# Optimization experiments

Hardware: AMD Instinct MI355X
Metric: run time of the kernel (lower is better)

## Reference

```python
import jax, jax.numpy as jnp
import numpy as np

B = 16384      # samples
NN = 11        # causal-graph nodes per sample (adult)
D = 4          # per-node raw feature dim (node_dim_max)
F = 32         # dim_input_enc = h_dim_list_enc[0]
EDIM = 4       # edge_dim
NI = 3         # number of intervention features

_BASE_EDGES = np.array([[0,3],[0,4],[1,3],[1,5],[2,5],[0,6],[3,6],[4,7],[5,7],
                        [6,8],[7,8],[2,9],[8,9],[3,10],[6,10],[9,10],[1,10]], dtype=np.int64)


def setup_inputs() -> dict:
    key = jax.random.key(0)
    ks = jax.random.split(key, 14)
    # batched edge index: replicate the 17-edge DAG per sample with node offsets
    off = (np.arange(B) * NN)[:, None]                      # [B,1]
    src = (_BASE_EDGES[:, 0][None, :] + off).reshape(-1).astype(np.int32)  # [E]
    dst = (_BASE_EDGES[:, 1][None, :] + off).reshape(-1).astype(np.int32)
    E = src.shape[0]
    g = lambda k, shp, s: jax.random.normal(k, shp, dtype=jnp.float32) * s
    return {
        'x_input':  g(ks[0], (B, NN * D), 1.0),
        'edge_attr': g(ks[1], (E, EDIM), 1.0),
        'W_emb':   g(ks[2], (NN, D, F), 1.0 / np.sqrt(D)),
        'b_emb':   jnp.zeros((NN, F), jnp.float32),
        'W_pre1':  g(ks[3], (NI, 2 * F + EDIM, F), 1.0 / np.sqrt(2 * F + EDIM)),
        'b_pre1':  jnp.zeros((NI, F), jnp.float32),
        'W_post1': g(ks[4], (NI, 12 * F, F), 1.0 / np.sqrt(12 * F)),
        'b_post1': jnp.zeros((NI, F), jnp.float32),
        'W_pre2':  g(ks[5], (NI, 2 * F + EDIM, F), 1.0 / np.sqrt(2 * F + EDIM)),
        'b_pre2':  jnp.zeros((NI, F), jnp.float32),
        'W_post2': g(ks[6], (NI, 12 * F, 1), 1.0 / np.sqrt(12 * F)),
        'b_post2': jnp.zeros((NI, 1), jnp.float32),
        'W_fc':    g(ks[7], (NI, NN, 1), 1.0 / np.sqrt(NN)),
        'b_fc':    jnp.zeros((NI, 1), jnp.float32),
        'edge_src': jnp.asarray(src),
        'edge_dst': jnp.asarray(dst),
    }


def _pna_conv(h, src, dst, e, Wpre, bpre, Wpost, bpost, cnt_c, mask, amp, att, N):
    # message: pre-MLP over [h_dst, h_src, edge_attr]
    m = jax.nn.relu(jnp.concatenate([h[dst], h[src], e], axis=1) @ Wpre + bpre)  # [E,F]
    s = jax.ops.segment_sum(m, dst, num_segments=N)
    mean = s / cnt_c[:, None]
    mean_sq = jax.ops.segment_sum(m * m, dst, num_segments=N) / cnt_c[:, None]
    std = jnp.sqrt(jax.nn.relu(mean_sq - mean * mean) + 1e-5)
    mn = jnp.where(mask[:, None], jax.ops.segment_min(m, dst, num_segments=N), 0.0)
    mx = jnp.where(mask[:, None], jax.ops.segment_max(m, dst, num_segments=N), 0.0)
    agg = jnp.concatenate([mean, mn, mx, std], axis=1)                 # [N,4F]
    scaled = jnp.concatenate([agg, agg * amp[:, None], agg * att[:, None]], axis=1)  # [N,12F]
    return scaled @ Wpost + bpost


def reference(x_input, edge_attr, W_emb, b_emb,
              W_pre1, b_pre1, W_post1, b_post1,
              W_pre2, b_pre2, W_post2, b_post2,
              W_fc, b_fc, edge_src, edge_dst):
    N = B * NN
    # encoder embeddings: per-node linear + relu (shared across interventions)
    X = x_input.reshape(B, NN, D)
    H = jax.nn.relu(jnp.einsum('bnd,ndf->bnf', X, W_emb) + b_emb).reshape(N, F)
    # degree stats for PNA scalers (in-degree)
    cnt = jax.ops.segment_sum(jnp.ones_like(edge_dst, dtype=jnp.float32), edge_dst, num_segments=N)
    mask = cnt > 0
    cnt_c = jnp.maximum(cnt, 1.0)
    logd = jnp.log1p(jnp.maximum(cnt, 1.0))
    avg_log = jnp.mean(logd)
    amp = logd / avg_log
    att = avg_log / logd
    outs = []
    for i in range(NI):
        h1 = jax.nn.relu(_pna_conv(H, edge_src, edge_dst, edge_attr,
                                   W_pre1[i], b_pre1[i], W_post1[i], b_post1[i],
                                   cnt_c, mask, amp, att, N))
        h2 = _pna_conv(h1, edge_src, edge_dst, edge_attr,
                       W_pre2[i], b_pre2[i], W_post2[i], b_post2[i],
                       cnt_c, mask, amp, att, N)            # [N,1]
        p = jax.nn.sigmoid(h2)                               # get_prob=True
        pm = p.reshape(B, NN).mean(axis=0)                   # return_mean=True -> [11]
        outs.append(pm @ W_fc[i] + b_fc[i])                  # [1]
    # padded sum over interventions == concatenation when inter_features == intervention_features
    return jnp.concatenate(outs)[None, :]                    # [1, NI]
```

## Files before the change

kernel.cpp:

```cpp
#include <hip/hip_runtime.h>
#include <math.h>

#define B_TOT   16384
#define SB      5
#define TPB     512

#define SSTRIDE 1868
#define OFF_H   0
#define OFF_EA  396
#define OFF_M   464
#define OFF_H1  OFF_M
#define OFF_AGG 1076
#define OFF_TD  OFF_AGG
#define OFF_TS  (OFF_AGG + 396)
#define OFF_A4  600
#define OFF_A10 640
#define WLDS    (SB * SSTRIDE)

#define L_WC1  0
#define L_B4   3072
#define L_H1C  3104
#define L_V1C1 3136
#define L_V10  3232
#define L_V4   3360
#define L_C42  3392
#define LTAB   3396
#define G_W10  3396
#define G_W4   7492
#define WTAB   8520
#define WS_TAB 64
#define LDS_FLOATS (WLDS + LTAB)
#define AVG_LOG 0.9976091242438673f

__constant__ int C_ESRC[17] = {0,0,1,1,2,0,3,4,5,6,7,2,8,3,6,9,1};
__constant__ int C_EDST[17] = {3,4,3,5,5,6,6,7,7,8,8,9,9,10,10,10,10};
__constant__ int C1EA[6] = {0,3,5,7,9,11};
__constant__ int C1EB[6] = {2,4,6,8,10,12};
__constant__ int C1N[6]  = {3,5,6,7,8,9};
__constant__ int CC1[8]  = {0,0,1,2,3,4,5,0};

#define FMA16(a, wb, u) do { \
    float4 w0_ = *(const float4*)(wb); \
    float4 w1_ = *(const float4*)((wb) + 32); \
    float4 w2_ = *(const float4*)((wb) + 64); \
    float4 w3_ = *(const float4*)((wb) + 96); \
    u.x = fmaf(a.x, w0_.x, u.x); u.y = fmaf(a.x, w0_.y, u.y); u.z = fmaf(a.x, w0_.z, u.z); u.w = fmaf(a.x, w0_.w, u.w); \
    u.x = fmaf(a.y, w1_.x, u.x); u.y = fmaf(a.y, w1_.y, u.y); u.z = fmaf(a.y, w1_.z, u.z); u.w = fmaf(a.y, w1_.w, u.w); \
    u.x = fmaf(a.z, w2_.x, u.x); u.y = fmaf(a.z, w2_.y, u.y); u.z = fmaf(a.z, w2_.z, u.z); u.w = fmaf(a.z, w2_.w, u.w); \
    u.x = fmaf(a.w, w3_.x, u.x); u.y = fmaf(a.w, w3_.y, u.y); u.z = fmaf(a.w, w3_.z, u.z); u.w = fmaf(a.w, w3_.w, u.w); \
} while (0)

static __device__ __forceinline__ float coef3(const float* __restrict__ W1, int r, int f, float amp, float att)
{
    return W1[r * 32 + f] + amp * W1[(128 + r) * 32 + f] + att * W1[(256 + r) * 32 + f];
}
static __device__ __forceinline__ float coef3s(const float* __restrict__ W2, int r, float amp, float att)
{
    return W2[r] + amp * W2[128 + r] + att * W2[256 + r];
}

extern "C" __global__ void pna_fold(const float* __restrict__ W_post1, const float* __restrict__ b_post1,
                                    const float* __restrict__ W_post2, const float* __restrict__ b_post2,
                                    float* __restrict__ ws)
{
    const int t0 = blockIdx.x * blockDim.x + threadIdx.x;
    const int NT = gridDim.x * blockDim.x;
    const float l1 = log1pf(1.f), l2 = log1pf(2.f), l4 = log1pf(4.f);
    const float amp1 = l1 / AVG_LOG, att1 = AVG_LOG / l1;
    const float amp2 = l2 / AVG_LOG, att2 = AVG_LOG / l2;
    const float amp4 = l4 / AVG_LOG, att4 = AVG_LOG / l4;
    const float SIG0 = 0.0031622776601683794f;

    for (int idx = t0; idx < 3 * WTAB; idx += NT) {
        const int i = idx / WTAB, off = idx % WTAB;
        const float* W1 = W_post1 + i * 384 * 32;
        const float* W2 = W_post2 + i * 384;
        float val = 0.f;
        if (off < 3072) {
            const int j = off >> 5, f = off & 31, sub = j >> 5, jj = j & 31;
            if (sub == 0)      val = coef3(W1, jj, f, amp2, att2) + 2.f * coef3(W1, 64 + jj, f, amp2, att2);
            else if (sub == 1) val = coef3(W1, 32 + jj, f, amp2, att2) - coef3(W1, 64 + jj, f, amp2, att2);
            else               val = coef3(W1, 96 + jj, f, amp2, att2);
        } else if (off < 3104) {
            const int f = off - 3072;
            float sum = 0.f;
            for (int jj = 0; jj < 32; ++jj) sum += coef3(W1, 96 + jj, f, amp1, att1);
            val = b_post1[i * 32 + f] + SIG0 * sum;
        } else if (off < 3136) {
            const int f = off - 3104;
            float sum = 0.f;
            for (int jj = 0; jj < 32; ++jj) sum += coef3(W1, 96 + jj, f, amp1, att1);
            val = fmaxf(b_post1[i * 32 + f] + SIG0 * sum, 0.f);
        } else if (off < 3232) {
            const int j = off - 3136, sub = j >> 5, jj = j & 31;
            if (sub == 0)      val = coef3s(W2, jj, amp2, att2) + 2.f * coef3s(W2, 64 + jj, amp2, att2);
            else if (sub == 1) val = coef3s(W2, 32 + jj, amp2, att2) - coef3s(W2, 64 + jj, amp2, att2);
            else               val = coef3s(W2, 96 + jj, amp2, att2);
        } else if (off < 3360) {
            val = coef3s(W2, off - 3232, amp4, att4);
        } else if (off < 3392) {
            const int jj = off - 3360;
            val = coef3s(W2, jj, amp1, att1) + coef3s(W2, 32 + jj, amp1, att1) + coef3s(W2, 64 + jj, amp1, att1);
        } else if (off == 3392) {
            float sum = 0.f;
            for (int jj = 0; jj < 32; ++jj) sum += coef3s(W2, 96 + jj, amp1, att1);
            val = SIG0 * sum;
        } else if (off >= G_W10 && off < G_W4) {
            const int rr = off - G_W10;
            val = coef3(W1, rr >> 5, rr & 31, amp4, att4);
        } else if (off >= G_W4 && off < G_W4 + 1024) {
            const int rr = off - G_W4;
            const int jj = rr >> 5, f = rr & 31;
            val = coef3(W1, jj, f, amp1, att1) + coef3(W1, 32 + jj, f, amp1, att1) + coef3(W1, 64 + jj, f, amp1, att1);
        }
        ws[WS_TAB + idx] = val;
    }
    if (t0 < 40) ws[t0] = 0.f;
    if (t0 >= 40 && t0 < 43) {
        const int i = t0 - 40;
        const float* W2 = W_post2 + i * 384;
        float sum = 0.f;
        for (int jj = 0; jj < 32; ++jj) sum += coef3s(W2, 96 + jj, amp1, att1);
        ws[40 + i] = 1.f / (1.f + expf(-(b_post2[i] + SIG0 * sum)));
    }
}

static __device__ __forceinline__ void conv_T(float* lds, int nsamp, int w, int lane, int hoff,
                                              const float* __restrict__ Wp,
                                              const float* __restrict__ bp)
{
    const int ty = w & 1;
    const int f0 = (w >> 1) * 8;
    const bool act = lane < nsamp * 11;
    const int cidx = act ? lane : 0;
    const int s = cidx / 11, n = cidx % 11;
    const float* Hrow = lds + s * SSTRIDE + hoff + n * 36;
    const float* wbase = Wp + ty * 32 * 32 + f0;
    float acc[8];
#pragma unroll
    for (int f = 0; f < 8; f++) acc[f] = ty ? 0.f : bp[f0 + f];
#pragma unroll
    for (int kq = 0; kq < 8; kq++) {
        float4 a = *(const float4*)(Hrow + kq * 4);
#pragma unroll
        for (int kk = 0; kk < 4; kk++) {
            float av = (kk == 0) ? a.x : (kk == 1) ? a.y : (kk == 2) ? a.z : a.w;
            const float* wr = wbase + (kq * 4 + kk) * 32;
#pragma unroll
            for (int f = 0; f < 8; f++) acc[f] = fmaf(av, wr[f], acc[f]);
        }
    }
    float* T = lds + s * SSTRIDE + (ty ? OFF_TS : OFF_TD) + n * 36 + f0;
    if (act) {
        *(float4*)(T + 0) = make_float4(acc[0], acc[1], acc[2], acc[3]);
        *(float4*)(T + 4) = make_float4(acc[4], acc[5], acc[6], acc[7]);
    }
}

static __device__ __forceinline__ void conv_combine(float* lds, int nsamp, int w, int lane,
                                                    const float* __restrict__ Wp)
{
    const int f0 = (w & 3) * 8, v = w >> 2;
    const int idx = v * 64 + lane;
    const bool act = idx < nsamp * 17;
    const int cidx = act ? idx : 0;
    const int s = cidx / 17, e = cidx % 17;
    float* S = lds + s * SSTRIDE;
    const int nd = C_EDST[e], ns = C_ESRC[e];
    float4 ev = *(const float4*)(S + OFF_EA + e * 4);
    const float* TD = S + OFF_TD + nd * 36 + f0;
    const float* TS = S + OFF_TS + ns * 36 + f0;
    float acc[8];
#pragma unroll
    for (int fq = 0; fq < 2; fq++) {
        float4 td = *(const float4*)(TD + fq * 4);
        float4 ts = *(const float4*)(TS + fq * 4);
        acc[fq*4+0] = td.x + ts.x; acc[fq*4+1] = td.y + ts.y;
        acc[fq*4+2] = td.z + ts.z; acc[fq*4+3] = td.w + ts.w;
    }
    const float* w64 = Wp + 64 * 32 + f0;
    const float* w65 = Wp + 65 * 32 + f0;
    const float* w66 = Wp + 66 * 32 + f0;
    const float* w67 = Wp + 67 * 32 + f0;
#pragma unroll
    for (int f = 0; f < 8; f++) {
        float a = acc[f];
        a = fmaf(ev.x, w64[f], a);
        a = fmaf(ev.y, w65[f], a);
        a = fmaf(ev.z, w66[f], a);
        a = fmaf(ev.w, w67[f], a);
        acc[f] = fmaxf(a, 0.f);
    }
    float* M = S + OFF_M + e * 36 + f0;
    if (act) {
        *(float4*)(M + 0) = make_float4(acc[0], acc[1], acc[2], acc[3]);
        *(float4*)(M + 4) = make_float4(acc[4], acc[5], acc[6], acc[7]);
    }
}

static __device__ __forceinline__ void agg_new(float* lds, int nsamp, int tid)
{
    if (tid >= nsamp * 64) return;
    const int s = tid >> 6, r = tid & 63;
    float* S = lds + s * SSTRIDE;
    const int q = r & 7, f = q * 4;
    if (r < 48) {
        const int c1 = r >> 3;
        float4 a = *(const float4*)(S + OFF_M + C1EA[c1] * 36 + f);
        float4 b = *(const float4*)(S + OFF_M + C1EB[c1] * 36 + f);
        float4 mean, mn, sd;
        mean.x = (a.x + b.x) * 0.5f; mean.y = (a.y + b.y) * 0.5f;
        mean.z = (a.z + b.z) * 0.5f; mean.w = (a.w + b.w) * 0.5f;
        mn.x = fminf(a.x, b.x); mn.y = fminf(a.y, b.y); mn.z = fminf(a.z, b.z); mn.w = fminf(a.w, b.w);
        float4 msq;
        msq.x = fmaf(b.x, b.x, a.x * a.x) * 0.5f;
        msq.y = fmaf(b.y, b.y, a.y * a.y) * 0.5f;
        msq.z = fmaf(b.z, b.z, a.z * a.z) * 0.5f;
        msq.w = fmaf(b.w, b.w, a.w * a.w) * 0.5f;
        sd.x = sqrtf(fmaxf(msq.x - mean.x * mean.x, 0.f) + 1e-5f);
        sd.y = sqrtf(fmaxf(msq.y - mean.y * mean.y, 0.f) + 1e-5f);
        sd.z = sqrtf(fmaxf(msq.z - mean.z * mean.z, 0.f) + 1e-5f);
        sd.w = sqrtf(fmaxf(msq.w - mean.w * mean.w, 0.f) + 1e-5f);
        float* A = S + OFF_AGG + c1 * 100;
        *(float4*)(A + f) = mean;
        *(float4*)(A + 32 + f) = mn;
        *(float4*)(A + 64 + f) = sd;
    } else if (r < 56) {
        *(float4*)(S + OFF_AGG + OFF_A4 + f) = *(const float4*)(S + OFF_M + 36 + f);
    } else {
        float4 sum = make_float4(0.f,0.f,0.f,0.f), sq = make_float4(0.f,0.f,0.f,0.f);
        float4 mn = make_float4(1e30f,1e30f,1e30f,1e30f), mx = make_float4(-1e30f,-1e30f,-1e30f,-1e30f);
#pragma unroll
        for (int e = 13; e <= 16; e++) {
            float4 mv = *(const float4*)(S + OFF_M + e * 36 + f);
            sum.x += mv.x; sum.y += mv.y; sum.z += mv.z; sum.w += mv.w;
            sq.x = fmaf(mv.x, mv.x, sq.x); sq.y = fmaf(mv.y, mv.y, sq.y);
            sq.z = fmaf(mv.z, mv.z, sq.z); sq.w = fmaf(mv.w, mv.w, sq.w);
            mn.x = fminf(mn.x, mv.x); mn.y = fminf(mn.y, mv.y); mn.z = fminf(mn.z, mv.z); mn.w = fminf(mn.w, mv.w);
            mx.x = fmaxf(mx.x, mv.x); mx.y = fmaxf(mx.y, mv.y); mx.z = fmaxf(mx.z, mv.z); mx.w = fmaxf(mx.w, mv.w);
        }
        float4 mean = make_float4(sum.x*0.25f, sum.y*0.25f, sum.z*0.25f, sum.w*0.25f);
        float4 msq  = make_float4(sq.x*0.25f,  sq.y*0.25f,  sq.z*0.25f,  sq.w*0.25f);
        float4 sd;
        sd.x = sqrtf(fmaxf(msq.x - mean.x*mean.x, 0.f) + 1e-5f);
        sd.y = sqrtf(fmaxf(msq.y - mean.y*mean.y, 0.f) + 1e-5f);
        sd.z = sqrtf(fmaxf(msq.z - mean.z*mean.z, 0.f) + 1e-5f);
        sd.w = sqrtf(fmaxf(msq.w - mean.w*mean.w, 0.f) + 1e-5f);
        float* A = S + OFF_AGG + OFF_A10;
        *(float4*)(A + f) = mean;
        *(float4*)(A + 32 + f) = mn;
        *(float4*)(A + 64 + f) = mx;
        *(float4*)(A + 96 + f) = sd;
    }
}

static __device__ __forceinline__ void post1_new(float* lds, const float* wl, int nsamp, int w, int lane,
                                                 const float* __restrict__ bp,
                                                 const float* __restrict__ tabg)
{
    if (w < 6) {
        const int t = w * 40 + lane;
        if (lane < 40 && t < nsamp * 48) {
            const int row = t >> 3, q = t & 7;
            const int s = row / 6, c1 = row - s * 6;
            const float* A = lds + s * SSTRIDE + OFF_AGG + c1 * 100;
            const float* W = wl + L_WC1 + q * 4;
            float4 u = make_float4(0.f,0.f,0.f,0.f);
#pragma unroll 4
            for (int jq = 0; jq < 24; ++jq) {
                float4 a = *(const float4*)(A + jq * 4);
                const float* wb = W + jq * 128;
                FMA16(a, wb, u);
            }
            float4 o;
            o.x = fmaxf(u.x + bp[q*4+0], 0.f);
            o.y = fmaxf(u.y + bp[q*4+1], 0.f);
            o.z = fmaxf(u.z + bp[q*4+2], 0.f);
            o.w = fmaxf(u.w + bp[q*4+3], 0.f);
            *(float4*)(lds + s * SSTRIDE + OFF_H1 + C1N[c1] * 36 + q * 4) = o;
        }
    } else if (w == 6) {
        if (lane < nsamp * 8) {
            const int s = lane >> 3, q = lane & 7;
            const float* A = lds + s * SSTRIDE + OFF_AGG + OFF_A10;
            const float* Wg = tabg + G_W10 + q * 4;
            float4 u = make_float4(0.f,0.f,0.f,0.f);
#pragma unroll 4
            for (int jq = 0; jq < 32; ++jq) {
                float4 a = *(const float4*)(A + jq * 4);
                const float* wb = Wg + jq * 128;
                FMA16(a, wb, u);
            }
            float4 o;
            o.x = fmaxf(u.x + bp[q*4+0], 0.f);
            o.y = fmaxf(u.y + bp[q*4+1], 0.f);
            o.z = fmaxf(u.z + bp[q*4+2], 0.f);
            o.w = fmaxf(u.w + bp[q*4+3], 0.f);
            *(float4*)(lds + s * SSTRIDE + OFF_H1 + 10 * 36 + q * 4) = o;
        }
    } else {
        if (lane < nsamp * 8) {
            const int s = lane >> 3, q = lane & 7;
            const float* A = lds + s * SSTRIDE + OFF_AGG + OFF_A4;
            const float* Wg = tabg + G_W4 + q * 4;
            float4 u = make_float4(0.f,0.f,0.f,0.f);
#pragma unroll
            for (int jq = 0; jq < 8; ++jq) {
                float4 a = *(const float4*)(A + jq * 4);
                const float* wb = Wg + jq * 128;
                FMA16(a, wb, u);
            }
            float4 b4 = *(const float4*)(wl + L_B4 + q * 4);
            float4 o;
            o.x = fmaxf(u.x + b4.x, 0.f);
            o.y = fmaxf(u.y + b4.y, 0.f);
            o.z = fmaxf(u.z + b4.z, 0.f);
            o.w = fmaxf(u.w + b4.w, 0.f);
            *(float4*)(lds + s * SSTRIDE + OFF_H1 + 4 * 36 + q * 4) = o;
        }
        for (int c = lane; c < nsamp * 24; c += 64) {
            const int s = c / 24, rr = c - s * 24, node = rr >> 3, q2 = rr & 7;
            *(float4*)(lds + s * SSTRIDE + OFF_H1 + node * 36 + q2 * 4) =
                *(const float4*)(wl + L_H1C + q2 * 4);
        }
    }
}

static __device__ __forceinline__ void post2_new(float* lds, const float* wl, int nsamp, int w, int lane,
                                                 float b2, float* __restrict__ gacc, int i)
{
    if (w != 0) return;
    float p = 0.f;
    if (lane < nsamp * 8) {
        const int s = lane >> 3, nn = lane & 7;
        const float* S = lds + s * SSTRIDE;
        const float* A; const float* V; int jqn; float extra = 0.f;
        if (nn == 1)      { A = S + OFF_AGG + OFF_A4;  V = wl + L_V4;  jqn = 8;  extra = wl[L_C42]; }
        else if (nn == 7) { A = S + OFF_AGG + OFF_A10; V = wl + L_V10; jqn = 32; }
        else              { A = S + OFF_AGG + CC1[nn] * 100; V = wl + L_V1C1; jqn = 24; }
        float u = 0.f;
        for (int jq = 0; jq < jqn; ++jq) {
            float4 a = *(const float4*)(A + jq * 4);
            float4 v = *(const float4*)(V + jq * 4);
            u = fmaf(a.x, v.x, u); u = fmaf(a.y, v.y, u);
            u = fmaf(a.z, v.z, u); u = fmaf(a.w, v.w, u);
        }
        const float h2 = u + b2 + extra;
        p = 1.f / (1.f + expf(-h2));
    }
    p += __shfl_down(p, 8);
    p += __shfl_down(p, 16);
    p += __shfl_down(p, 32);
    if (lane < 8) atomicAdd(gacc + i * 11 + 3 + lane, p);
}

extern "C" __global__ void __launch_bounds__(TPB, 6)
pna_main(const float* __restrict__ x_input, const float* __restrict__ edge_attr,
         const float* __restrict__ W_emb,  const float* __restrict__ b_emb,
         const float* __restrict__ W_pre1, const float* __restrict__ b_pre1,
         const float* __restrict__ b_post1,
         const float* __restrict__ W_pre2, const float* __restrict__ b_pre2,
         const float* __restrict__ b_post2,
         const float* __restrict__ wstab,  float* __restrict__ gacc)
{
    extern __shared__ float lds[];
    const int tid = threadIdx.x;
    const int w = __builtin_amdgcn_readfirstlane(tid >> 6);
    const int lane = tid & 63;
    const int s0 = blockIdx.x * SB;
    const int nsamp = min(SB, B_TOT - s0);
    float* wl = lds + WLDS;

    for (int t = tid; t < nsamp * 68; t += TPB)
        lds[(t / 68) * SSTRIDE + OFF_EA + (t % 68)] = edge_attr[(size_t)s0 * 68 + t];

    for (int t = tid; t < nsamp * 352; t += TPB) {
        const int s = t / 352, r = t % 352, n = r >> 5, f = r & 31;
        const float* Xs = x_input + (size_t)(s0 + s) * 44 + n * 4;
        const float* We = W_emb + (n * 4) * 32 + f;
        float v = b_emb[n * 32 + f];
        v = fmaf(Xs[0], We[0],  v);
        v = fmaf(Xs[1], We[32], v);
        v = fmaf(Xs[2], We[64], v);
        v = fmaf(Xs[3], We[96], v);
        lds[s * SSTRIDE + OFF_H + n * 36 + f] = fmaxf(v, 0.f);
    }
    __syncthreads();

    for (int i = 0; i < 3; i++) {
        const float* tab = wstab + i * WTAB;
        for (int t = tid; t < LTAB / 4; t += TPB)
            ((float4*)wl)[t] = ((const float4*)tab)[t];
        conv_T(lds, nsamp, w, lane, OFF_H, W_pre1 + i * 68 * 32, b_pre1 + i * 32);
        __syncthreads();
        conv_combine(lds, nsamp, w, lane, W_pre1 + i * 68 * 32);
        __syncthreads();
        agg_new(lds, nsamp, tid);
        __syncthreads();
        post1_new(lds, wl, nsamp, w, lane, b_post1 + i * 32, tab);
        __syncthreads();
        conv_T(lds, nsamp, w, lane, OFF_H1, W_pre2 + i * 68 * 32, b_pre2 + i * 32);
        __syncthreads();
        conv_combine(lds, nsamp, w, lane, W_pre2 + i * 68 * 32);
        __syncthreads();
        agg_new(lds, nsamp, tid);
        __syncthreads();
        post2_new(lds, wl, nsamp, w, lane, b_post2[i], gacc, i);
        __syncthreads();
    }
}

extern "C" __global__ void pna_final(const float* __restrict__ ws,
                                     const float* __restrict__ W_fc,
                                     const float* __restrict__ b_fc,
                                     float* __restrict__ out)
{
    const int i = threadIdx.x;
    if (i < 3) {
        float acc = 0.f;
        for (int n = 0; n < 11; n++)
            acc = fmaf(ws[i * 11 + n] * (1.f / 16384.f), W_fc[i * 11 + n], acc);
        const float pc = ws[40 + i];
        const float wsum = W_fc[i * 11 + 0] + W_fc[i * 11 + 1] + W_fc[i * 11 + 2];
        out[i] = acc + pc * wsum + b_fc[i];
    }
}

extern "C" void kernel_launch(void* const* d_in, const int* in_sizes, int n_in,
                              void* d_out, int out_size, void* d_ws, size_t ws_size,
                              hipStream_t stream)
{
    (void)in_sizes; (void)n_in; (void)out_size; (void)ws_size;
    const float* x_input   = (const float*)d_in[0];
    const float* edge_attr = (const float*)d_in[1];
    const float* W_emb     = (const float*)d_in[2];
    const float* b_emb     = (const float*)d_in[3];
    const float* W_pre1    = (const float*)d_in[4];
    const float* b_pre1    = (const float*)d_in[5];
    const float* W_post1   = (const float*)d_in[6];
    const float* b_post1   = (const float*)d_in[7];
    const float* W_pre2    = (const float*)d_in[8];
    const float* b_pre2    = (const float*)d_in[9];
    const float* W_post2   = (const float*)d_in[10];
    const float* b_post2   = (const float*)d_in[11];
    const float* W_fc      = (const float*)d_in[12];
    const float* b_fc      = (const float*)d_in[13];
    float* ws  = (float*)d_ws;
    float* out = (float*)d_out;

    hipLaunchKernelGGL(pna_fold, dim3(64), dim3(512), 0, stream,
                       W_post1, b_post1, W_post2, b_post2, ws);
    const int grid = (B_TOT + SB - 1) / SB;
    const size_t shmem = (size_t)LDS_FLOATS * sizeof(float);
    hipLaunchKernelGGL(pna_main, dim3(grid), dim3(TPB), shmem, stream,
                       x_input, edge_attr, W_emb, b_emb,
                       W_pre1, b_pre1, b_post1,
                       W_pre2, b_pre2, b_post2,
                       ws + WS_TAB, ws);
    hipLaunchKernelGGL(pna_final, dim3(1), dim3(64), 0, stream, ws, W_fc, b_fc, out);
}
```

Baseline: 351.5 us.

## Fuse message, aggregation and post2 stages; shrink LDS layout and accumulate probabilities locally

```diff
diff --git a/kernel.cpp b/kernel.cpp
--- a/kernel.cpp
+++ b/kernel.cpp
@@ -5,39 +5,43 @@
 #define SB      5
 #define TPB     512
 
-#define SSTRIDE 1868
+#define SSTRIDE 1652
 #define OFF_H   0
 #define OFF_EA  396
-#define OFF_M   464
-#define OFF_H1  OFF_M
-#define OFF_AGG 1076
+#define OFF_H1  464
+#define OFF_AGG 860
 #define OFF_TD  OFF_AGG
 #define OFF_TS  (OFF_AGG + 396)
 #define OFF_A4  600
 #define OFF_A10 640
 #define WLDS    (SB * SSTRIDE)
 
-#define L_WC1  0
-#define L_B4   3072
-#define L_H1C  3104
-#define L_V1C1 3136
-#define L_V10  3232
-#define L_V4   3360
-#define L_C42  3392
-#define LTAB   3396
-#define G_W10  3396
-#define G_W4   7492
+#define LW_B4   0
+#define LW_H1C  32
+#define LW_V1C1 64
+#define LW_V10  160
+#define LW_V4   288
+#define LW_C42  320
+#define LW_BP1  324
+#define LW_EA1  356
+#define LW_EA2  484
+#define LTAB    612
+
+#define OFF_PACC (WLDS + LTAB)
+#define LDS_FLOATS (WLDS + LTAB + 16)
+
+#define G_WC1  0
+#define G_W10  3072
+#define G_W4   7168
+#define G_SM   8192
 #define WTAB   8520
 #define WS_TAB 64
-#define LDS_FLOATS (WLDS + LTAB)
 #define AVG_LOG 0.9976091242438673f
 
 __constant__ int C_ESRC[17] = {0,0,1,1,2,0,3,4,5,6,7,2,8,3,6,9,1};
-__constant__ int C_EDST[17] = {3,4,3,5,5,6,6,7,7,8,8,9,9,10,10,10,10};
 __constant__ int C1EA[6] = {0,3,5,7,9,11};
 __constant__ int C1EB[6] = {2,4,6,8,10,12};
 __constant__ int C1N[6]  = {3,5,6,7,8,9};
-__constant__ int CC1[8]  = {0,0,1,2,3,4,5,0};
 
 #define FMA16(a, wb, u) do { \
     float4 w0_ = *(const float4*)(wb); \
@@ -50,9 +54,20 @@
     u.x = fmaf(a.w, w3_.x, u.x); u.y = fmaf(a.w, w3_.y, u.y); u.z = fmaf(a.w, w3_.z, u.z); u.w = fmaf(a.w, w3_.w, u.w); \
 } while (0)
 
-static __device__ __forceinline__ float coef3(const float* __restrict__ W1, int r, int f, float amp, float att)
-{
-    return W1[r * 32 + f] + amp * W1[(128 + r) * 32 + f] + att * W1[(256 + r) * 32 + f];
+#define MSG(e_, m_) do { \
+    const float4 ev_ = *(const float4*)(S + OFF_EA + (e_) * 4); \
+    const float4 ts_ = *(const float4*)(S + OFF_TS + C_ESRC[(e_)] * 36 + f); \
+    m_.x = base.x + ts_.x; m_.y = base.y + ts_.y; m_.z = base.z + ts_.z; m_.w = base.w + ts_.w; \
+    m_.x = fmaf(ev_.x, w0.x, m_.x); m_.y = fmaf(ev_.x, w0.y, m_.y); m_.z = fmaf(ev_.x, w0.z, m_.z); m_.w = fmaf(ev_.x, w0.w, m_.w); \
+    m_.x = fmaf(ev_.y, w1.x, m_.x); m_.y = fmaf(ev_.y, w1.y, m_.y); m_.z = fmaf(ev_.y, w1.z, m_.z); m_.w = fmaf(ev_.y, w1.w, m_.w); \
+    m_.x = fmaf(ev_.z, w2.x, m_.x); m_.y = fmaf(ev_.z, w2.y, m_.y); m_.z = fmaf(ev_.z, w2.z, m_.z); m_.w = fmaf(ev_.z, w2.w, m_.w); \
+    m_.x = fmaf(ev_.w, w3.x, m_.x); m_.y = fmaf(ev_.w, w3.y, m_.y); m_.z = fmaf(ev_.w, w3.z, m_.z); m_.w = fmaf(ev_.w, w3.w, m_.w); \
+    m_.x = fmaxf(m_.x, 0.f); m_.y = fmaxf(m_.y, 0.f); m_.z = fmaxf(m_.z, 0.f); m_.w = fmaxf(m_.w, 0.f); \
+} while (0)
+
+static __device__ __forceinline__ float coef3(const float* __restrict__ W1, int r, int fcol, float amp, float att)
+{
+    return W1[r * 32 + fcol] + amp * W1[(128 + r) * 32 + fcol] + att * W1[(256 + r) * 32 + fcol];
 }
 static __device__ __forceinline__ float coef3s(const float* __restrict__ W2, int r, float amp, float att)
 {
@@ -77,41 +92,41 @@
         const float* W2 = W_post2 + i * 384;
         float val = 0.f;
         if (off < 3072) {
-            const int j = off >> 5, f = off & 31, sub = j >> 5, jj = j & 31;
-            if (sub == 0)      val = coef3(W1, jj, f, amp2, att2) + 2.f * coef3(W1, 64 + jj, f, amp2, att2);
-            else if (sub == 1) val = coef3(W1, 32 + jj, f, amp2, att2) - coef3(W1, 64 + jj, f, amp2, att2);
-            else               val = coef3(W1, 96 + jj, f, amp2, att2);
-        } else if (off < 3104) {
-            const int f = off - 3072;
-            float sum = 0.f;
-            for (int jj = 0; jj < 32; ++jj) sum += coef3(W1, 96 + jj, f, amp1, att1);
-            val = b_post1[i * 32 + f] + SIG0 * sum;
-        } else if (off < 3136) {
-            const int f = off - 3104;
-            float sum = 0.f;
-            for (int jj = 0; jj < 32; ++jj) sum += coef3(W1, 96 + jj, f, amp1, att1);
-            val = fmaxf(b_post1[i * 32 + f] + SIG0 * sum, 0.f);
-        } else if (off < 3232) {
-            const int j = off - 3136, sub = j >> 5, jj = j & 31;
+            const int j = off >> 5, fcol = off & 31, sub = j >> 5, jj = j & 31;
+            if (sub == 0)      val = coef3(W1, jj, fcol, amp2, att2) + 2.f * coef3(W1, 64 + jj, fcol, amp2, att2);
+            else if (sub == 1) val = coef3(W1, 32 + jj, fcol, amp2, att2) - coef3(W1, 64 + jj, fcol, amp2, att2);
+            else               val = coef3(W1, 96 + jj, fcol, amp2, att2);
+        } else if (off < 7168) {
+            const int rr = off - 3072;
+            val = coef3(W1, rr >> 5, rr & 31, amp4, att4);
+        } else if (off < 8192) {
+            const int rr = off - 7168, jj = rr >> 5, fcol = rr & 31;
+            val = coef3(W1, jj, fcol, amp1, att1) + coef3(W1, 32 + jj, fcol, amp1, att1)
+                + coef3(W1, 64 + jj, fcol, amp1, att1);
+        } else if (off < 8224) {
+            const int fcol = off - 8192;
+            float ssum = 0.f;
+            for (int jj = 0; jj < 32; ++jj) ssum += coef3(W1, 96 + jj, fcol, amp1, att1);
+            val = b_post1[i * 32 + fcol] + SIG0 * ssum;
+        } else if (off < 8256) {
+            const int fcol = off - 8224;
+            float ssum = 0.f;
+            for (int jj = 0; jj < 32; ++jj) ssum += coef3(W1, 96 + jj, fcol, amp1, att1);
+            val = fmaxf(b_post1[i * 32 + fcol] + SIG0 * ssum, 0.f);
+        } else if (off < 8352) {
+            const int j = off - 8256, sub = j >> 5, jj = j & 31;
             if (sub == 0)      val = coef3s(W2, jj, amp2, att2) + 2.f * coef3s(W2, 64 + jj, amp2, att2);
             else if (sub == 1) val = coef3s(W2, 32 + jj, amp2, att2) - coef3s(W2, 64 + jj, amp2, att2);
             else               val = coef3s(W2, 96 + jj, amp2, att2);
-        } else if (off < 3360) {
-            val = coef3s(W2, off - 3232, amp4, att4);
-        } else if (off < 3392) {
-            const int jj = off - 3360;
+        } else if (off < 8480) {
+            val = coef3s(W2, off - 8352, amp4, att4);
+        } else if (off < 8512) {
+            const int jj = off - 8480;
             val = coef3s(W2, jj, amp1, att1) + coef3s(W2, 32 + jj, amp1, att1) + coef3s(W2, 64 + jj, amp1, att1);
-        } else if (off == 3392) {
-            float sum = 0.f;
-            for (int jj = 0; jj < 32; ++jj) sum += coef3s(W2, 96 + jj, amp1, att1);
-            val = SIG0 * sum;
-        } else if (off >= G_W10 && off < G_W4) {
-            const int rr = off - G_W10;
-            val = coef3(W1, rr >> 5, rr & 31, amp4, att4);
-        } else if (off >= G_W4 && off < G_W4 + 1024) {
-            const int rr = off - G_W4;
-            const int jj = rr >> 5, f = rr & 31;
-            val = coef3(W1, jj, f, amp1, att1) + coef3(W1, 32 + jj, f, amp1, att1) + coef3(W1, 64 + jj, f, amp1, att1);
+        } else if (off == 8512) {
+            float ssum = 0.f;
+            for (int jj = 0; jj < 32; ++jj) ssum += coef3s(W2, 96 + jj, amp1, att1);
+            val = SIG0 * ssum;
         }
         ws[WS_TAB + idx] = val;
     }
@@ -119,9 +134,9 @@
     if (t0 >= 40 && t0 < 43) {
         const int i = t0 - 40;
         const float* W2 = W_post2 + i * 384;
-        float sum = 0.f;
-        for (int jj = 0; jj < 32; ++jj) sum += coef3s(W2, 96 + jj, amp1, att1);
-        ws[40 + i] = 1.f / (1.f + expf(-(b_post2[i] + SIG0 * sum)));
+        float ssum = 0.f;
+        for (int jj = 0; jj < 32; ++jj) ssum += coef3s(W2, 96 + jj, amp1, att1);
+        ws[40 + i] = 1.f / (1.f + expf(-(b_post2[i] + SIG0 * ssum)));
     }
 }
 
@@ -157,204 +172,185 @@
     }
 }
 
-static __device__ __forceinline__ void conv_combine(float* lds, int nsamp, int w, int lane,
-                                                    const float* __restrict__ Wp)
-{
-    const int f0 = (w & 3) * 8, v = w >> 2;
-    const int idx = v * 64 + lane;
-    const bool act = idx < nsamp * 17;
-    const int cidx = act ? idx : 0;
-    const int s = cidx / 17, e = cidx % 17;
+template<int CONV2>
+static __device__ __forceinline__ void fused_conv(float* lds, const float* wl, int nsamp,
+                                                  int w, int lane, float b2, float* pacc)
+{
+    const bool act = lane < nsamp * 8;
+    const int l = act ? lane : 0;
+    const int s = l >> 3, q = l & 7, f = q * 4;
     float* S = lds + s * SSTRIDE;
-    const int nd = C_EDST[e], ns = C_ESRC[e];
-    float4 ev = *(const float4*)(S + OFF_EA + e * 4);
-    const float* TD = S + OFF_TD + nd * 36 + f0;
-    const float* TS = S + OFF_TS + ns * 36 + f0;
-    float acc[8];
-#pragma unroll
-    for (int fq = 0; fq < 2; fq++) {
-        float4 td = *(const float4*)(TD + fq * 4);
-        float4 ts = *(const float4*)(TS + fq * 4);
-        acc[fq*4+0] = td.x + ts.x; acc[fq*4+1] = td.y + ts.y;
-        acc[fq*4+2] = td.z + ts.z; acc[fq*4+3] = td.w + ts.w;
-    }
-    const float* w64 = Wp + 64 * 32 + f0;
-    const float* w65 = Wp + 65 * 32 + f0;
-    const float* w66 = Wp + 66 * 32 + f0;
-    const float* w67 = Wp + 67 * 32 + f0;
-#pragma unroll
-    for (int f = 0; f < 8; f++) {
-        float a = acc[f];
-        a = fmaf(ev.x, w64[f], a);
-        a = fmaf(ev.y, w65[f], a);
-        a = fmaf(ev.z, w66[f], a);
-        a = fmaf(ev.w, w67[f], a);
-        acc[f] = fmaxf(a, 0.f);
-    }
-    float* M = S + OFF_M + e * 36 + f0;
-    if (act) {
-        *(float4*)(M + 0) = make_float4(acc[0], acc[1], acc[2], acc[3]);
-        *(float4*)(M + 4) = make_float4(acc[4], acc[5], acc[6], acc[7]);
-    }
-}
-
-static __device__ __forceinline__ void agg_new(float* lds, int nsamp, int tid)
-{
-    if (tid >= nsamp * 64) return;
-    const int s = tid >> 6, r = tid & 63;
-    float* S = lds + s * SSTRIDE;
-    const int q = r & 7, f = q * 4;
-    if (r < 48) {
-        const int c1 = r >> 3;
-        float4 a = *(const float4*)(S + OFF_M + C1EA[c1] * 36 + f);
-        float4 b = *(const float4*)(S + OFF_M + C1EB[c1] * 36 + f);
-        float4 mean, mn, sd;
-        mean.x = (a.x + b.x) * 0.5f; mean.y = (a.y + b.y) * 0.5f;
-        mean.z = (a.z + b.z) * 0.5f; mean.w = (a.w + b.w) * 0.5f;
-        mn.x = fminf(a.x, b.x); mn.y = fminf(a.y, b.y); mn.z = fminf(a.z, b.z); mn.w = fminf(a.w, b.w);
+    const float* WE = wl + (CONV2 ? LW_EA2 : LW_EA1) + f;
+    const float4 w0 = *(const float4*)(WE);
+    const float4 w1 = *(const float4*)(WE + 32);
+    const float4 w2 = *(const float4*)(WE + 64);
+    const float4 w3 = *(const float4*)(WE + 96);
+
+    float4 r0 = make_float4(0.f,0.f,0.f,0.f), r1 = r0, r2 = r0, r3 = r0;
+    float u = 0.f;
+
+    if (w < 6) {
+        const int n = C1N[w];
+        float4 base = *(const float4*)(S + OFF_TD + n * 36 + f);
+        float4 ma, mb;
+        MSG(C1EA[w], ma);
+        MSG(C1EB[w], mb);
+        r0.x = (ma.x + mb.x) * 0.5f; r0.y = (ma.y + mb.y) * 0.5f;
+        r0.z = (ma.z + mb.z) * 0.5f; r0.w = (ma.w + mb.w) * 0.5f;
+        r1.x = fminf(ma.x, mb.x); r1.y = fminf(ma.y, mb.y);
+        r1.z = fminf(ma.z, mb.z); r1.w = fminf(ma.w, mb.w);
         float4 msq;
-        msq.x = fmaf(b.x, b.x, a.x * a.x) * 0.5f;
-        msq.y = fmaf(b.y, b.y, a.y * a.y) * 0.5f;
-        msq.z = fmaf(b.z, b.z, a.z * a.z) * 0.5f;
-        msq.w = fmaf(b.w, b.w, a.w * a.w) * 0.5f;
-        sd.x = sqrtf(fmaxf(msq.x - mean.x * mean.x, 0.f) + 1e-5f);
-        sd.y = sqrtf(fmaxf(msq.y - mean.y * mean.y, 0.f) + 1e-5f);
-        sd.z = sqrtf(fmaxf(msq.z - mean.z * mean.z, 0.f) + 1e-5f);
-        sd.w = sqrtf(fmaxf(msq.w - mean.w * mean.w, 0.f) + 1e-5f);
-        float* A = S + OFF_AGG + c1 * 100;
-        *(float4*)(A + f) = mean;
-        *(float4*)(A + 32 + f) = mn;
-        *(float4*)(A + 64 + f) = sd;
-    } else if (r < 56) {
-        *(float4*)(S + OFF_AGG + OFF_A4 + f) = *(const float4*)(S + OFF_M + 36 + f);
+        msq.x = fmaf(mb.x, mb.x, ma.x * ma.x) * 0.5f;
+        msq.y = fmaf(mb.y, mb.y, ma.y * ma.y) * 0.5f;
+        msq.z = fmaf(mb.z, mb.z, ma.z * ma.z) * 0.5f;
+        msq.w = fmaf(mb.w, mb.w, ma.w * ma.w) * 0.5f;
+        r2.x = sqrtf(fmaxf(msq.x - r0.x * r0.x, 0.f) + 1e-5f);
+        r2.y = sqrtf(fmaxf(msq.y - r0.y * r0.y, 0.f) + 1e-5f);
+        r2.z = sqrtf(fmaxf(msq.z - r0.z * r0.z, 0.f) + 1e-5f);
+        r2.w = sqrtf(fmaxf(msq.w - r0.w * r0.w, 0.f) + 1e-5f);
+        if (CONV2) {
+            const float* V = wl + LW_V1C1 + f;
+            const float4 v0 = *(const float4*)(V);
+            const float4 v1 = *(const float4*)(V + 32);
+            const float4 v2 = *(const float4*)(V + 64);
+            u = fmaf(r0.x, v0.x, fmaf(r0.y, v0.y, fmaf(r0.z, v0.z, r0.w * v0.w)));
+            u = fmaf(r1.x, v1.x, fmaf(r1.y, v1.y, fmaf(r1.z, v1.z, fmaf(r1.w, v1.w, u))));
+            u = fmaf(r2.x, v2.x, fmaf(r2.y, v2.y, fmaf(r2.z, v2.z, fmaf(r2.w, v2.w, u))));
+        }
+    } else if (w == 6) {
+        float4 base = *(const float4*)(S + OFF_TD + 4 * 36 + f);
+        float4 m;
+        MSG(1, m);
+        r0 = m;
+        if (CONV2) {
+            const float4 v0 = *(const float4*)(wl + LW_V4 + f);
+            u = fmaf(m.x, v0.x, fmaf(m.y, v0.y, fmaf(m.z, v0.z, m.w * v0.w)));
+        }
     } else {
-        float4 sum = make_float4(0.f,0.f,0.f,0.f), sq = make_float4(0.f,0.f,0.f,0.f);
-        float4 mn = make_float4(1e30f,1e30f,1e30f,1e30f), mx = make_float4(-1e30f,-1e30f,-1e30f,-1e30f);
-#pragma unroll
-        for (int e = 13; e <= 16; e++) {
-            float4 mv = *(const float4*)(S + OFF_M + e * 36 + f);
-            sum.x += mv.x; sum.y += mv.y; sum.z += mv.z; sum.w += mv.w;
-            sq.x = fmaf(mv.x, mv.x, sq.x); sq.y = fmaf(mv.y, mv.y, sq.y);
-            sq.z = fmaf(mv.z, mv.z, sq.z); sq.w = fmaf(mv.w, mv.w, sq.w);
-            mn.x = fminf(mn.x, mv.x); mn.y = fminf(mn.y, mv.y); mn.z = fminf(mn.z, mv.z); mn.w = fminf(mn.w, mv.w);
-            mx.x = fmaxf(mx.x, mv.x); mx.y = fmaxf(mx.y, mv.y); mx.z = fmaxf(mx.z, mv.z); mx.w = fmaxf(mx.w, mv.w);
-        }
-        float4 mean = make_float4(sum.x*0.25f, sum.y*0.25f, sum.z*0.25f, sum.w*0.25f);
-        float4 msq  = make_float4(sq.x*0.25f,  sq.y*0.25f,  sq.z*0.25f,  sq.w*0.25f);
-        float4 sd;
-        sd.x = sqrtf(fmaxf(msq.x - mean.x*mean.x, 0.f) + 1e-5f);
-        sd.y = sqrtf(fmaxf(msq.y - mean.y*mean.y, 0.f) + 1e-5f);
-        sd.z = sqrtf(fmaxf(msq.z - mean.z*mean.z, 0.f) + 1e-5f);
-        sd.w = sqrtf(fmaxf(msq.w - mean.w*mean.w, 0.f) + 1e-5f);
-        float* A = S + OFF_AGG + OFF_A10;
-        *(float4*)(A + f) = mean;
-        *(float4*)(A + 32 + f) = mn;
-        *(float4*)(A + 64 + f) = mx;
-        *(float4*)(A + 96 + f) = sd;
+        float4 base = *(const float4*)(S + OFF_TD + 10 * 36 + f);
+        float4 sum = make_float4(0.f,0.f,0.f,0.f), sq = sum;
+        float4 mn = make_float4(1e30f,1e30f,1e30f,1e30f);
+        float4 mx = make_float4(-1e30f,-1e30f,-1e30f,-1e30f);
+#pragma unroll
+        for (int e = 13; e <= 16; ++e) {
+            float4 m;
+            MSG(e, m);
+            sum.x += m.x; sum.y += m.y; sum.z += m.z; sum.w += m.w;
+            sq.x = fmaf(m.x, m.x, sq.x); sq.y = fmaf(m.y, m.y, sq.y);
+            sq.z = fmaf(m.z, m.z, sq.z); sq.w = fmaf(m.w, m.w, sq.w);
+            mn.x = fminf(mn.x, m.x); mn.y = fminf(mn.y, m.y); mn.z = fminf(mn.z, m.z); mn.w = fminf(mn.w, m.w);
+            mx.x = fmaxf(mx.x, m.x); mx.y = fmaxf(mx.y, m.y); mx.z = fmaxf(mx.z, m.z); mx.w = fmaxf(mx.w, m.w);
+        }
+        r0.x = sum.x * 0.25f; r0.y = sum.y * 0.25f; r0.z = sum.z * 0.25f; r0.w = sum.w * 0.25f;
+        r1 = mn; r2 = mx;
+        float4 msq = make_float4(sq.x * 0.25f, sq.y * 0.25f, sq.z * 0.25f, sq.w * 0.25f);
+        r3.x = sqrtf(fmaxf(msq.x - r0.x * r0.x, 0.f) + 1e-5f);
+        r3.y = sqrtf(fmaxf(msq.y - r0.y * r0.y, 0.f) + 1e-5f);
+        r3.z = sqrtf(fmaxf(msq.z - r0.z * r0.z, 0.f) + 1e-5f);
+        r3.w = sqrtf(fmaxf(msq.w - r0.w * r0.w, 0.f) + 1e-5f);
+        if (CONV2) {
+            const float* V = wl + LW_V10 + f;
+            const float4 v0 = *(const float4*)(V);
+            const float4 v1 = *(const float4*)(V + 32);
+            const float4 v2 = *(const float4*)(V + 64);
+            const float4 v3 = *(const float4*)(V + 96);
+            u = fmaf(r0.x, v0.x, fmaf(r0.y, v0.y, fmaf(r0.z, v0.z, r0.w * v0.w)));
+            u = fmaf(r1.x, v1.x, fmaf(r1.y, v1.y, fmaf(r1.z, v1.z, fmaf(r1.w, v1.w, u))));
+            u = fmaf(r2.x, v2.x, fmaf(r2.y, v2.y, fmaf(r2.z, v2.z, fmaf(r2.w, v2.w, u))));
+            u = fmaf(r3.x, v3.x, fmaf(r3.y, v3.y, fmaf(r3.z, v3.z, fmaf(r3.w, v3.w, u))));
+        }
+    }
+
+    if (!CONV2) {
+        __syncthreads();
+        if (act) {
+            if (w < 6) {
+                float* A = S + OFF_AGG + w * 100;
+                *(float4*)(A + f) = r0; *(float4*)(A + 32 + f) = r1; *(float4*)(A + 64 + f) = r2;
+            } else if (w == 6) {
+                *(float4*)(S + OFF_AGG + OFF_A4 + f) = r0;
+            } else {
+                float* A = S + OFF_AGG + OFF_A10;
+                *(float4*)(A + f) = r0; *(float4*)(A + 32 + f) = r1;
+                *(float4*)(A + 64 + f) = r2; *(float4*)(A + 96 + f) = r3;
+            }
+        }
+    } else {
+        u += __shfl_xor(u, 1);
+        u += __shfl_xor(u, 2);
+        u += __shfl_xor(u, 4);
+        if (act && q == 0) {
+            const float extra = (w == 6) ? wl[LW_C42] : 0.f;
+            const int node = (w < 6) ? C1N[w] : (w == 6 ? 4 : 10);
+            const float p = 1.f / (1.f + expf(-(u + b2 + extra)));
+            atomicAdd(pacc + node, p);
+        }
     }
 }
 
 static __device__ __forceinline__ void post1_new(float* lds, const float* wl, int nsamp, int w, int lane,
-                                                 const float* __restrict__ bp,
                                                  const float* __restrict__ tabg)
 {
+    const bool act = lane < nsamp * 8;
+    const int l = act ? lane : 0;
+    const int s = l >> 3, q = l & 7;
     if (w < 6) {
-        const int t = w * 40 + lane;
-        if (lane < 40 && t < nsamp * 48) {
-            const int row = t >> 3, q = t & 7;
-            const int s = row / 6, c1 = row - s * 6;
-            const float* A = lds + s * SSTRIDE + OFF_AGG + c1 * 100;
-            const float* W = wl + L_WC1 + q * 4;
-            float4 u = make_float4(0.f,0.f,0.f,0.f);
-#pragma unroll 4
-            for (int jq = 0; jq < 24; ++jq) {
-                float4 a = *(const float4*)(A + jq * 4);
-                const float* wb = W + jq * 128;
-                FMA16(a, wb, u);
-            }
+        const float* A = lds + s * SSTRIDE + OFF_AGG + w * 100;
+        const float* W = tabg + G_WC1 + q * 4;
+        float4 u = make_float4(0.f,0.f,0.f,0.f);
+#pragma unroll 2
+        for (int jq = 0; jq < 24; ++jq) {
+            float4 a = *(const float4*)(A + jq * 4);
+            FMA16(a, W + jq * 128, u);
+        }
+        if (act) {
+            const float4 b = *(const float4*)(wl + LW_BP1 + q * 4);
             float4 o;
-            o.x = fmaxf(u.x + bp[q*4+0], 0.f);
-            o.y = fmaxf(u.y + bp[q*4+1], 0.f);
-            o.z = fmaxf(u.z + bp[q*4+2], 0.f);
-            o.w = fmaxf(u.w + bp[q*4+3], 0.f);
-            *(float4*)(lds + s * SSTRIDE + OFF_H1 + C1N[c1] * 36 + q * 4) = o;
+            o.x = fmaxf(u.x + b.x, 0.f); o.y = fmaxf(u.y + b.y, 0.f);
+            o.z = fmaxf(u.z + b.z, 0.f); o.w = fmaxf(u.w + b.w, 0.f);
+            *(float4*)(lds + s * SSTRIDE + OFF_H1 + C1N[w] * 36 + q * 4) = o;
         }
     } else if (w == 6) {
-        if (lane < nsamp * 8) {
-            const int s = lane >> 3, q = lane & 7;
-            const float* A = lds + s * SSTRIDE + OFF_AGG + OFF_A10;
-            const float* Wg = tabg + G_W10 + q * 4;
-            float4 u = make_float4(0.f,0.f,0.f,0.f);
-#pragma unroll 4
-            for (int jq = 0; jq < 32; ++jq) {
-                float4 a = *(const float4*)(A + jq * 4);
-                const float* wb = Wg + jq * 128;
-                FMA16(a, wb, u);
-            }
+        const float* A = lds + s * SSTRIDE + OFF_AGG + OFF_A10;
+        const float* W = tabg + G_W10 + q * 4;
+        float4 u = make_float4(0.f,0.f,0.f,0.f);
+#pragma unroll 2
+        for (int jq = 0; jq < 32; ++jq) {
+            float4 a = *(const float4*)(A + jq * 4);
+            FMA16(a, W + jq * 128, u);
+        }
+        if (act) {
+            const float4 b = *(const float4*)(wl + LW_BP1 + q * 4);
             float4 o;
-            o.x = fmaxf(u.x + bp[q*4+0], 0.f);
-            o.y = fmaxf(u.y + bp[q*4+1], 0.f);
-            o.z = fmaxf(u.z + bp[q*4+2], 0.f);
-            o.w = fmaxf(u.w + bp[q*4+3], 0.f);
+            o.x = fmaxf(u.x + b.x, 0.f); o.y = fmaxf(u.y + b.y, 0.f);
+            o.z = fmaxf(u.z + b.z, 0.f); o.w = fmaxf(u.w + b.w, 0.f);
             *(float4*)(lds + s * SSTRIDE + OFF_H1 + 10 * 36 + q * 4) = o;
         }
     } else {
-        if (lane < nsamp * 8) {
-            const int s = lane >> 3, q = lane & 7;
-            const float* A = lds + s * SSTRIDE + OFF_AGG + OFF_A4;
-            const float* Wg = tabg + G_W4 + q * 4;
-            float4 u = make_float4(0.f,0.f,0.f,0.f);
-#pragma unroll
-            for (int jq = 0; jq < 8; ++jq) {
-                float4 a = *(const float4*)(A + jq * 4);
-                const float* wb = Wg + jq * 128;
-                FMA16(a, wb, u);
-            }
-            float4 b4 = *(const float4*)(wl + L_B4 + q * 4);
+        const float* A = lds + s * SSTRIDE + OFF_AGG + OFF_A4;
+        const float* W = tabg + G_W4 + q * 4;
+        float4 u = make_float4(0.f,0.f,0.f,0.f);
+#pragma unroll
+        for (int jq = 0; jq < 8; ++jq) {
+            float4 a = *(const float4*)(A + jq * 4);
+            FMA16(a, W + jq * 128, u);
+        }
+        if (act) {
+            const float4 b = *(const float4*)(wl + LW_B4 + q * 4);
             float4 o;
-            o.x = fmaxf(u.x + b4.x, 0.f);
-            o.y = fmaxf(u.y + b4.y, 0.f);
-            o.z = fmaxf(u.z + b4.z, 0.f);
-            o.w = fmaxf(u.w + b4.w, 0.f);
+            o.x = fmaxf(u.x + b.x, 0.f); o.y = fmaxf(u.y + b.y, 0.f);
+            o.z = fmaxf(u.z + b.z, 0.f); o.w = fmaxf(u.w + b.w, 0.f);
             *(float4*)(lds + s * SSTRIDE + OFF_H1 + 4 * 36 + q * 4) = o;
         }
         for (int c = lane; c < nsamp * 24; c += 64) {
-            const int s = c / 24, rr = c - s * 24, node = rr >> 3, q2 = rr & 7;
-            *(float4*)(lds + s * SSTRIDE + OFF_H1 + node * 36 + q2 * 4) =
-                *(const float4*)(wl + L_H1C + q2 * 4);
-        }
-    }
-}
-
-static __device__ __forceinline__ void post2_new(float* lds, const float* wl, int nsamp, int w, int lane,
-                                                 float b2, float* __restrict__ gacc, int i)
-{
-    if (w != 0) return;
-    float p = 0.f;
-    if (lane < nsamp * 8) {
-        const int s = lane >> 3, nn = lane & 7;
-        const float* S = lds + s * SSTRIDE;
-        const float* A; const float* V; int jqn; float extra = 0.f;
-        if (nn == 1)      { A = S + OFF_AGG + OFF_A4;  V = wl + L_V4;  jqn = 8;  extra = wl[L_C42]; }
-        else if (nn == 7) { A = S + OFF_AGG + OFF_A10; V = wl + L_V10; jqn = 32; }
-        else              { A = S + OFF_AGG + CC1[nn] * 100; V = wl + L_V1C1; jqn = 24; }
-        float u = 0.f;
-        for (int jq = 0; jq < jqn; ++jq) {
-            float4 a = *(const float4*)(A + jq * 4);
-            float4 v = *(const float4*)(V + jq * 4);
-            u = fmaf(a.x, v.x, u); u = fmaf(a.y, v.y, u);
-            u = fmaf(a.z, v.z, u); u = fmaf(a.w, v.w, u);
-        }
-        const float h2 = u + b2 + extra;
-        p = 1.f / (1.f + expf(-h2));
-    }
-    p += __shfl_down(p, 8);
-    p += __shfl_down(p, 16);
-    p += __shfl_down(p, 32);
-    if (lane < 8) atomicAdd(gacc + i * 11 + 3 + lane, p);
-}
-
-extern "C" __global__ void __launch_bounds__(TPB, 6)
+            const int cs = c / 24, rr = c - cs * 24, node = rr >> 3, q2 = rr & 7;
+            *(float4*)(lds + cs * SSTRIDE + OFF_H1 + node * 36 + q2 * 4) =
+                *(const float4*)(wl + LW_H1C + q2 * 4);
+        }
+    }
+}
+
+extern "C" __global__ void __launch_bounds__(TPB, 8)
 pna_main(const float* __restrict__ x_input, const float* __restrict__ edge_attr,
          const float* __restrict__ W_emb,  const float* __restrict__ b_emb,
          const float* __restrict__ W_pre1, const float* __restrict__ b_pre1,
@@ -370,6 +366,9 @@
     const int s0 = blockIdx.x * SB;
     const int nsamp = min(SB, B_TOT - s0);
     float* wl = lds + WLDS;
+    float* pacc = lds + OFF_PACC;
+
+    if (tid < 16) pacc[tid] = 0.f;
 
     for (int t = tid; t < nsamp * 68; t += TPB)
         lds[(t / 68) * SSTRIDE + OFF_EA + (t % 68)] = edge_attr[(size_t)s0 * 68 + t];
@@ -389,24 +388,25 @@
 
     for (int i = 0; i < 3; i++) {
         const float* tab = wstab + i * WTAB;
-        for (int t = tid; t < LTAB / 4; t += TPB)
-            ((float4*)wl)[t] = ((const float4*)tab)[t];
-        conv_T(lds, nsamp, w, lane, OFF_H, W_pre1 + i * 68 * 32, b_pre1 + i * 32);
-        __syncthreads();
-        conv_combine(lds, nsamp, w, lane, W_pre1 + i * 68 * 32);
-        __syncthreads();
-        agg_new(lds, nsamp, tid);
-        __syncthreads();
-        post1_new(lds, wl, nsamp, w, lane, b_post1 + i * 32, tab);
-        __syncthreads();
-        conv_T(lds, nsamp, w, lane, OFF_H1, W_pre2 + i * 68 * 32, b_pre2 + i * 32);
-        __syncthreads();
-        conv_combine(lds, nsamp, w, lane, W_pre2 + i * 68 * 32);
-        __syncthreads();
-        agg_new(lds, nsamp, tid);
-        __syncthreads();
-        post2_new(lds, wl, nsamp, w, lane, b_post2[i], gacc, i);
-        __syncthreads();
+        if (tid < 81)       ((float4*)wl)[tid] = ((const float4*)(tab + G_SM))[tid];
+        else if (tid < 89)  ((float4*)(wl + LW_BP1))[tid - 81] = ((const float4*)(b_post1 + i * 32))[tid - 81];
+        else if (tid < 121) ((float4*)(wl + LW_EA1))[tid - 89] = ((const float4*)(W_pre1 + i * 2176 + 2048))[tid - 89];
+        else if (tid < 153) ((float4*)(wl + LW_EA2))[tid - 121] = ((const float4*)(W_pre2 + i * 2176 + 2048))[tid - 121];
+
+        conv_T(lds, nsamp, w, lane, OFF_H, W_pre1 + i * 2176, b_pre1 + i * 32);
+        __syncthreads();
+        fused_conv<0>(lds, wl, nsamp, w, lane, 0.f, pacc);
+        __syncthreads();
+        post1_new(lds, wl, nsamp, w, lane, tab);
+        __syncthreads();
+        conv_T(lds, nsamp, w, lane, OFF_H1, W_pre2 + i * 2176, b_pre2 + i * 32);
+        __syncthreads();
+        fused_conv<1>(lds, wl, nsamp, w, lane, b_post2[i], pacc);
+        __syncthreads();
+        if (tid < 11) {
+            atomicAdd(gacc + i * 11 + tid, pacc[tid]);
+            pacc[tid] = 0.f;
+        }
     }
 }
 
```

New measurement: 405.5 us. +15.4%, slower.
